# Performance work log

Hardware: AMD Instinct MI355X
Metric: run time of the kernel (lower is better)

Reference implementation:

```python
import jax, jax.numpy as jnp
import numpy as np

H = 128       # hidden size
IN = 6        # input size
OUT = 1       # output size
B, T = 128, 2048


def setup_inputs() -> dict:
    key = jax.random.key(0)
    ks = jax.random.split(key, 16)
    s = 1.0 / np.sqrt(H)  # PyTorch LSTM init: U(-1/sqrt(H), 1/sqrt(H))
    u = lambda k, shape: jax.random.uniform(k, shape, jnp.float32, -s, s)
    inp = {"x": jax.random.normal(ks[0], (B, T, IN), jnp.float32)}
    in_sizes = [IN, H, H]
    for l in range(3):
        inp[f"W_ih{l}"] = u(ks[1 + 4 * l], (4 * H, in_sizes[l]))
        inp[f"W_hh{l}"] = u(ks[2 + 4 * l], (4 * H, H))
        inp[f"b_ih{l}"] = u(ks[3 + 4 * l], (4 * H,))
        inp[f"b_hh{l}"] = u(ks[4 + 4 * l], (4 * H,))
    inp["W_out"] = u(ks[13], (OUT, H))
    inp["b_out"] = u(ks[14], (OUT,))
    return inp


def _lstm_layer(x, W_ih, W_hh, b):
    # x: [B, T, D_in]; precompute input contribution once, scan the recurrence.
    xg = jnp.einsum("bti,gi->btg", x, W_ih) + b  # [B, T, 4H]
    h0 = jnp.zeros((x.shape[0], H), x.dtype)
    c0 = jnp.zeros((x.shape[0], H), x.dtype)

    def step(carry, xg_t):
        h, c = carry
        g = xg_t + h @ W_hh.T                     # [B, 4H]
        i, f, gg, o = jnp.split(g, 4, axis=-1)    # PyTorch gate order i,f,g,o
        i = jax.nn.sigmoid(i)
        f = jax.nn.sigmoid(f)
        gg = jnp.tanh(gg)
        o = jax.nn.sigmoid(o)
        c = f * c + i * gg
        h = o * jnp.tanh(c)
        return (h, c), h

    _, hs = jax.lax.scan(step, (h0, c0), jnp.swapaxes(xg, 0, 1))  # hs: [T, B, H]
    return jnp.swapaxes(hs, 0, 1)


def reference(x, W_ih0, W_hh0, b_ih0, b_hh0, W_ih1, W_hh1, b_ih1, b_hh1,
              W_ih2, W_hh2, b_ih2, b_hh2, W_out, b_out):
    # 3-layer LSTM (dropout inactive in eval mode) + linear head on last step.
    h = _lstm_layer(x, W_ih0, W_hh0, b_ih0 + b_hh0)
    h = _lstm_layer(h, W_ih1, W_hh1, b_ih1 + b_hh1)
    h = _lstm_layer(h, W_ih2, W_hh2, b_ih2 + b_hh2)
    return h[:, -1, :] @ W_out.T + b_out  # [B, 1]
```

## Files before the change

### kernel.cpp

```cpp
#include <hip/hip_runtime.h>

#define B_ 128
#define T_ 2048
#define H_ 128
#define IN_ 6
#define GRP_ 8
#define NGRP_ (T_ / GRP_)
#define CHUNK_ 32
#define NCHUNK_ (T_ / CHUNK_)
#define FLAG_STRIDE_ 64
#define HS_ 144
#define XGRING_ 3
#define XGSLOT_ (CHUNK_ * 8192)

typedef _Float16 f16x8 __attribute__((ext_vector_type(8)));
typedef float    f32x4 __attribute__((ext_vector_type(4)));

__device__ __forceinline__ unsigned short f2h_u(float f) {
  union { _Float16 h; unsigned short u; } v; v.h = (_Float16)f; return v.u;
}
__device__ __forceinline__ unsigned int pack2(float a, float b) {
  return (unsigned int)f2h_u(a) | ((unsigned int)f2h_u(b) << 16);
}
__device__ __forceinline__ float sigf_(float x) {
  return __builtin_amdgcn_rcpf(1.0f + __expf(-x));
}
__device__ __forceinline__ float tanhf_(float x) {
  return 2.0f * __builtin_amdgcn_rcpf(1.0f + __expf(-2.0f * x)) - 1.0f;
}
__device__ __forceinline__ f16x8 load_w8(const float* __restrict__ p) {
  f16x8 r;
#pragma unroll
  for (int i = 0; i < 8; ++i) r[i] = (_Float16)p[i];
  return r;
}

__global__ void init_flags(unsigned int* flags) {
  flags[blockIdx.x * 256 + threadIdx.x] = 0u;
}

__global__ __launch_bounds__(512, 2)
void lstm_pipe(const float* __restrict__ x,
               const float* __restrict__ Wih0, const float* __restrict__ Whh0,
               const float* __restrict__ bih0, const float* __restrict__ bhh0,
               const float* __restrict__ Wih1, const float* __restrict__ Whh1,
               const float* __restrict__ bih1, const float* __restrict__ bhh1,
               const float* __restrict__ Wih2, const float* __restrict__ Whh2,
               const float* __restrict__ bih2, const float* __restrict__ bhh2,
               unsigned short* __restrict__ region,
               float* __restrict__ xg,
               unsigned int* __restrict__ state_h,
               unsigned int* __restrict__ flags)
{
  const int bid  = blockIdx.x;
  const int tid  = threadIdx.x;
  const int lane = tid & 63;
  const int wv   = tid >> 6;
  const int n16  = lane & 15;
  const int quad = lane >> 4;
  const int bcol = n16 & 7;
  const int hh   = n16 >> 3;

  __shared__ unsigned short smem[32 * 16 * HS_];
  __shared__ int s_have;

#define WAITP(ptr_, need_, have_)                                   \
  do {                                                              \
    if ((have_) < (need_)) {                                        \
      if (tid == 0) {                                               \
        int v = (int)__hip_atomic_load(ptr_, __ATOMIC_RELAXED,      \
                                       __HIP_MEMORY_SCOPE_AGENT);   \
        while (v < (need_)) {                                       \
          __builtin_amdgcn_s_sleep(2);                              \
          v = (int)__hip_atomic_load(ptr_, __ATOMIC_RELAXED,        \
                                     __HIP_MEMORY_SCOPE_AGENT);     \
        }                                                           \
        (void)__hip_atomic_load(ptr_, __ATOMIC_ACQUIRE,             \
                                __HIP_MEMORY_SCOPE_AGENT);          \
        s_have = v;                                                 \
      }                                                             \
      __syncthreads();                                              \
      (have_) = s_have;                                             \
    }                                                               \
  } while (0)

  if (bid >= 48) {
    const int gi = bid - 48;
    const int gl = 1 + (gi >> 3);
    const int bg = gi & 7;
    const float* Wih = (gl == 1) ? Wih1 : Wih2;
    const float* bih = (gl == 1) ? bih1 : bih2;
    const float* bhh = (gl == 1) ? bhh1 : bhh2;
    float* xgo = xg + (size_t)((gl - 1) * 8 + bg) * (XGRING_ * (size_t)XGSLOT_);
    unsigned int* fhA = &flags[((gl - 1) * 16 + 2 * bg)     * FLAG_STRIDE_];
    unsigned int* fhB = &flags[((gl - 1) * 16 + 2 * bg + 1) * FLAG_STRIDE_];
    unsigned int* fx_out = &flags[(32 + (gl - 1) * 8 + bg) * FLAG_STRIDE_];
    unsigned int* fcA = &flags[(48 + (gl - 1) * 16 + 2 * bg)     * FLAG_STRIDE_];
    unsigned int* fcB = &flags[(48 + (gl - 1) * 16 + 2 * bg + 1) * FLAG_STRIDE_];

    f16x8 wih[4][4];
#pragma unroll
    for (int j = 0; j < 4; ++j)
#pragma unroll
      for (int kc = 0; kc < 4; ++kc)
        wih[j][kc] = load_w8(Wih + (size_t)(j * 128 + 16 * wv + n16) * H_ + kc * 32 + quad * 8);
    f32x4 bias4[4];
#pragma unroll
    for (int j = 0; j < 4; ++j)
#pragma unroll
      for (int r = 0; r < 4; ++r) {
        int row = j * 128 + 16 * wv + quad * 4 + r;
        bias4[j][r] = bih[row] + bhh[row];
      }

    int haveA = 0, haveB = 0, havecA = 0, havecB = 0;
    const int tt = tid >> 4, bb = tid & 15;
    const int swk = bb & 7;
    for (int k = 0; k < NCHUNK_; ++k) {
      WAITP(fhA, k + 1, haveA);
      WAITP(fhB, k + 1, haveB);
      if (k >= XGRING_) {
        WAITP(fcA, k - (XGRING_ - 1), havecA);
        WAITP(fcB, k - (XGRING_ - 1), havecB);
      }
      {
        const uint4* gp = (const uint4*)(region +
            ((size_t)(bg * 16 + bb) * T_ + (size_t)(CHUNK_ * k + tt)) * H_);
        uint4* lp = (uint4*)&smem[(tt * 16 + bb) * HS_];
#pragma unroll
        for (int i = 0; i < 16; ++i) lp[i ^ swk] = gp[i];
      }
      __syncthreads();
      const int slot = k % XGRING_;
      for (int t = 0; t < CHUNK_; ++t) {
        f16x8 hi[4];
#pragma unroll
        for (int kc = 0; kc < 4; ++kc)
          hi[kc] = *(const f16x8*)&smem[(t * 16 + n16) * HS_ +
                                        ((kc * 32 + quad * 8) ^ (bcol << 3))];
        float* xp = xgo + (size_t)(slot * CHUNK_ + t) * 8192 + quad * 64 + n16 * 4;
#pragma unroll
        for (int j = 0; j < 4; ++j) {
          f32x4 a = bias4[j];
#pragma unroll
          for (int kc = 0; kc < 4; ++kc)
            a = __builtin_amdgcn_mfma_f32_16x16x32_f16(wih[j][kc], hi[kc], a, 0, 0, 0);
          *(f32x4*)(xp + (size_t)(8 * j + wv) * 256) = a;
        }
      }
      __syncthreads();
      if (tid == 0)
        __hip_atomic_store(fx_out, (unsigned int)(k + 1),
                           __ATOMIC_RELEASE, __HIP_MEMORY_SCOPE_AGENT);
    }
    return;
  }

  const int layer = bid >> 4;
  const int bgg   = bid & 15;
  const int bg    = bgg >> 1;
  const int half  = bgg & 1;
  const int batch = bg * 16 + half * 8 + bcol;
  const float* Whh = (layer == 0) ? Whh0 : ((layer == 1) ? Whh1 : Whh2);

  unsigned short* hstate = smem;
  unsigned short* xb = smem + 2 * 8 * HS_;

  f16x8 whh[4][4];
#pragma unroll
  for (int j = 0; j < 4; ++j)
#pragma unroll
    for (int kc = 0; kc < 4; ++kc)
      whh[j][kc] = load_w8(Whh + (size_t)(j * 128 + 16 * wv + n16) * H_ + kc * 32 + quad * 8);

  for (int i = tid; i < (2 * 8 * HS_) / 2; i += 512) ((unsigned int*)smem)[i] = 0u;

  float c20 = 0.f, c21 = 0.f;
  unsigned int dh[GRP_];
  unsigned int* fh_out = (layer < 2) ? &flags[(layer * 16 + bgg) * FLAG_STRIDE_] : nullptr;
  const int hu_idx = (8 * wv + 2 * quad + hh) ^ (bcol << 2);
  const int hcol   = 16 * wv + 4 * quad + 2 * hh;

  if (layer == 0) {
    f32x4 bias4[4];
#pragma unroll
    for (int j = 0; j < 4; ++j)
#pragma unroll
      for (int r = 0; r < 4; ++r) {
        int row = j * 128 + 16 * wv + quad * 4 + r;
        bias4[j][r] = bih0[row] + bhh0[row];
      }
    f16x8 wx[4];
#pragma unroll
    for (int j = 0; j < 4; ++j)
#pragma unroll
      for (int i = 0; i < 8; ++i) wx[j][i] = (_Float16)0.f;
    if (quad == 0) {
#pragma unroll
      for (int j = 0; j < 4; ++j) {
        const float* p = Wih0 + (size_t)(j * 128 + 16 * wv + n16) * IN_;
#pragma unroll
        for (int i = 0; i < IN_; ++i) wx[j][i] = (_Float16)p[i];
      }
    }
    const f32x4 z4 = {0.f, 0.f, 0.f, 0.f};
    const int sn_x = tid & 7, st_x = tid >> 3;
    uint4 xreg = {0u, 0u, 0u, 0u};
    __syncthreads();
    if (tid < 64) {
      const float* xp = x + ((size_t)(bg * 16 + half * 8 + sn_x) * T_ + st_x) * IN_;
      xreg.x = pack2(xp[0], xp[1]); xreg.y = pack2(xp[2], xp[3]);
      xreg.z = pack2(xp[4], xp[5]); xreg.w = 0u;
      *(uint4*)&xb[(st_x * 8 + sn_x) * 8] = xreg;
    }
    __syncthreads();

    for (int g = 0; g < NGRP_; ++g) {
      int gs = (g + 1 < NGRP_) ? (g + 1) : g;
      if (tid < 64) {
        const float* xp = x + ((size_t)(bg * 16 + half * 8 + sn_x) * T_ + (8 * gs + st_x)) * IN_;
        xreg.x = pack2(xp[0], xp[1]); xreg.y = pack2(xp[2], xp[3]);
        xreg.z = pack2(xp[4], xp[5]); xreg.w = 0u;
      }
#pragma unroll
      for (int s = 0; s < GRP_; ++s) {
        const int rp = s & 1, wp = rp ^ 1;
        f16x8 hs[4];
#pragma unroll
        for (int kc = 0; kc < 4; ++kc)
          hs[kc] = *(const f16x8*)&hstate[(rp * 8 + bcol) * HS_ +
                                          ((kc * 32 + quad * 8) ^ (bcol << 3))];
        f16x8 xi;
#pragma unroll
        for (int i = 0; i < 8; ++i) xi[i] = (_Float16)0.f;
        if (quad == 0) xi = *(const f16x8*)&xb[(s * 8 + bcol) * 8];
        f32x4 acc[4];
#pragma unroll
        for (int j = 0; j < 4; ++j) {
          f32x4 aw = bias4[j];
#pragma unroll
          for (int kc = 0; kc < 4; ++kc)
            aw = __builtin_amdgcn_mfma_f32_16x16x32_f16(whh[j][kc], hs[kc], aw, 0, 0, 0);
          f32x4 ai = __builtin_amdgcn_mfma_f32_16x16x32_f16(wx[j], xi, z4, 0, 0, 0);
#pragma unroll
          for (int r = 0; r < 4; ++r) acc[j][r] = aw[r] + ai[r];
        }
        float ga[4], gb[4];
#pragma unroll
        for (int j = 0; j < 4; ++j) {
          ga[j] = hh ? acc[j][2] : acc[j][0];
          gb[j] = hh ? acc[j][3] : acc[j][1];
        }
        float i0 = sigf_(ga[0]), f0 = sigf_(ga[1]), t0 = tanhf_(ga[2]), o0 = sigf_(ga[3]);
        c20 = f0 * c20 + i0 * t0;
        float h0 = o0 * tanhf_(c20);
        float i1 = sigf_(gb[0]), f1 = sigf_(gb[1]), t1 = tanhf_(gb[2]), o1 = sigf_(gb[3]);
        c21 = f1 * c21 + i1 * t1;
        float h1 = o1 * tanhf_(c21);
        unsigned int u = pack2(h0, h1);
        dh[s] = u;
        ((unsigned int*)&hstate[(wp * 8 + bcol) * HS_])[hu_idx] = u;
        __syncthreads();
      }
#pragma unroll
      for (int s = 0; s < GRP_; ++s) {
        size_t off = ((size_t)batch * T_ + (8 * g + s)) * H_ + hcol;
        *(unsigned int*)(region + off) = dh[s];
      }
      if (tid < 64) *(uint4*)&xb[(st_x * 8 + sn_x) * 8] = xreg;
      __syncthreads();
      if (((g & 3) == 3) && tid == 0)
        __hip_atomic_store(fh_out, (unsigned int)((g >> 2) + 1),
                           __ATOMIC_RELEASE, __HIP_MEMORY_SCOPE_AGENT);
    }
  } else {
    const float* xgi = xg + (size_t)((layer - 1) * 8 + bg) * (XGRING_ * (size_t)XGSLOT_);
    const int xcol = half * 8 + bcol;
    f32x4 xr[2][4];
    auto load_xg = [&](int t, int buf) {
      int slot = (t >> 5) % XGRING_;
      const float* p = xgi + (size_t)(slot * CHUNK_ + (t & 31)) * 8192
                       + (size_t)wv * 256 + quad * 64 + xcol * 4;
      xr[buf][0] = *(const f32x4*)(p);
      xr[buf][1] = *(const f32x4*)(p + 2048);
      xr[buf][2] = *(const f32x4*)(p + 4096);
      xr[buf][3] = *(const f32x4*)(p + 6144);
    };
    unsigned int* fx_in  = &flags[(32 + (layer - 1) * 8 + bg) * FLAG_STRIDE_];
    unsigned int* fc_out = &flags[(48 + (layer - 1) * 16 + bgg) * FLAG_STRIDE_];
    int have_x = 0;
    __syncthreads();

    for (int g = 0; g < NGRP_; ++g) {
      if ((g & 3) == 0) {
        int c = g >> 2;
        WAITP(fx_in, c + 1, have_x);
        load_xg(32 * c, 0);
        load_xg(32 * c + 1, 1);
      }
#pragma unroll
      for (int s = 0; s < GRP_; ++s) {
        const int t = 8 * g + s;
        const int rp = s & 1, wp = rp ^ 1;
        f16x8 hs[4];
#pragma unroll
        for (int kc = 0; kc < 4; ++kc)
          hs[kc] = *(const f16x8*)&hstate[(rp * 8 + bcol) * HS_ +
                                          ((kc * 32 + quad * 8) ^ (bcol << 3))];
        f32x4 ci[4];
#pragma unroll
        for (int j = 0; j < 4; ++j) ci[j] = xr[s & 1][j];
        if (!(((g & 3) == 3) && s >= 6)) load_xg(t + 2, s & 1);
        f32x4 acc[4];
#pragma unroll
        for (int j = 0; j < 4; ++j) {
          f32x4 aw = ci[j];
#pragma unroll
          for (int kc = 0; kc < 4; ++kc)
            aw = __builtin_amdgcn_mfma_f32_16x16x32_f16(whh[j][kc], hs[kc], aw, 0, 0, 0);
          acc[j] = aw;
        }
        float ga[4], gb[4];
#pragma unroll
        for (int j = 0; j < 4; ++j) {
          ga[j] = hh ? acc[j][2] : acc[j][0];
          gb[j] = hh ? acc[j][3] : acc[j][1];
        }
        float i0 = sigf_(ga[0]), f0 = sigf_(ga[1]), t0 = tanhf_(ga[2]), o0 = sigf_(ga[3]);
        c20 = f0 * c20 + i0 * t0;
        float h0 = o0 * tanhf_(c20);
        float i1 = sigf_(gb[0]), f1 = sigf_(gb[1]), t1 = tanhf_(gb[2]), o1 = sigf_(gb[3]);
        c21 = f1 * c21 + i1 * t1;
        float h1 = o1 * tanhf_(c21);
        unsigned int u = pack2(h0, h1);
        dh[s] = u;
        ((unsigned int*)&hstate[(wp * 8 + bcol) * HS_])[hu_idx] = u;
        __syncthreads();
      }
      if (layer == 1) {
#pragma unroll
        for (int s = 0; s < GRP_; ++s) {
          size_t off = ((size_t)batch * T_ + (8 * g + s)) * H_ + hcol;
          *(unsigned int*)(region + off) = dh[s];
        }
        __syncthreads();
      }
      if (((g & 3) == 3) && tid == 0) {
        unsigned int cdone = (unsigned int)((g >> 2) + 1);
        if (layer == 1)
          __hip_atomic_store(fh_out, cdone, __ATOMIC_RELEASE, __HIP_MEMORY_SCOPE_AGENT);
        __hip_atomic_store(fc_out, cdone, __ATOMIC_RELEASE, __HIP_MEMORY_SCOPE_AGENT);
      }
    }
    if (layer == 2)
      state_h[(size_t)batch * 64 + (8 * wv + 2 * quad + hh)] = dh[GRP_ - 1];
  }
#undef WAITP
}

__global__ void head_kernel(const unsigned int* __restrict__ state_h,
                            const float* __restrict__ Wout,
                            const float* __restrict__ bout,
                            float* __restrict__ out)
{
  int b = threadIdx.x;
  float s = bout[0];
  for (int j = 0; j < 64; ++j) {
    unsigned int p = state_h[b * 64 + j];
    union { unsigned short u; _Float16 h; } lo, hi;
    lo.u = (unsigned short)(p & 0xffffu);
    hi.u = (unsigned short)(p >> 16);
    s += (float)lo.h * Wout[2 * j] + (float)hi.h * Wout[2 * j + 1];
  }
  out[b] = s;
}

extern "C" void kernel_launch(void* const* d_in, const int* in_sizes, int n_in,
                              void* d_out, int out_size, void* d_ws, size_t ws_size,
                              hipStream_t stream)
{
  const float* x = (const float*)d_in[0];
  const float* Wih[3] = {(const float*)d_in[1], (const float*)d_in[5], (const float*)d_in[9]};
  const float* Whh[3] = {(const float*)d_in[2], (const float*)d_in[6], (const float*)d_in[10]};
  const float* bih[3] = {(const float*)d_in[3], (const float*)d_in[7], (const float*)d_in[11]};
  const float* bhh[3] = {(const float*)d_in[4], (const float*)d_in[8], (const float*)d_in[12]};
  const float* Wout = (const float*)d_in[13];
  const float* bout = (const float*)d_in[14];
  float* out = (float*)d_out;

  char* ws = (char*)d_ws;
  size_t off = 0;
  unsigned short* region = (unsigned short*)(ws + off); off += (size_t)B_ * T_ * H_ * 2;
  float* xg = (float*)(ws + off);                       off += (size_t)16 * XGRING_ * XGSLOT_ * 4;
  unsigned int* state_h  = (unsigned int*)(ws + off);   off += (size_t)B_ * 64 * 4;
  off = (off + 255) & ~(size_t)255;
  unsigned int* flags    = (unsigned int*)(ws + off);   off += 80 * FLAG_STRIDE_ * 4;

  init_flags<<<20, 256, 0, stream>>>(flags);
  lstm_pipe<<<64, 512, 0, stream>>>(x,
      Wih[0], Whh[0], bih[0], bhh[0],
      Wih[1], Whh[1], bih[1], bhh[1],
      Wih[2], Whh[2], bih[2], bhh[2],
      region, xg, state_h, flags);
  head_kernel<<<1, 128, 0, stream>>>(state_h, Wout, bout, out);
}
```

Baseline: 1.790 ms.

## Split recurrent batch into 4-sample slices across twice as many blocks

Each recurrent block now handles 4 batch rows instead of 8, so the 48 recurrent blocks become 96 (32 per layer). Each lane now computes one hidden unit instead of two, which halves per-step gate math and the serial latency per step. The step barriers are replaced with a raw lgkmcnt wait plus s_barrier, and an explicit vmcnt fence is added before flag publication. Layer 0 also folds the input MFMA into the accumulation chain as its first term. In exchange the MFMA tiles are only a quarter used on the batch dimension, there are more flags to poll, and more blocks compete for CUs.

Result: faster. 1.541 ms (-13.9%).

```diff
diff --git a/kernel.cpp b/kernel.cpp
--- a/kernel.cpp
+++ b/kernel.cpp
@@ -12,6 +12,8 @@
 #define HS_ 144
 #define XGRING_ 3
 #define XGSLOT_ (CHUNK_ * 8192)
+#define NSLICE_ 32
+#define NFLAGS_ 144
 
 typedef _Float16 f16x8 __attribute__((ext_vector_type(8)));
 typedef float    f32x4 __attribute__((ext_vector_type(4)));
@@ -38,6 +40,19 @@
 __global__ void init_flags(unsigned int* flags) {
   flags[blockIdx.x * 256 + threadIdx.x] = 0u;
 }
+
+#define BARRIER_LGKM()                                              \
+  do {                                                              \
+    asm volatile("s_waitcnt lgkmcnt(0)" ::: "memory");              \
+    __builtin_amdgcn_s_barrier();                                   \
+    __builtin_amdgcn_sched_barrier(0);                              \
+  } while (0)
+
+#define PUBLISH_FENCE()                                             \
+  do {                                                              \
+    asm volatile("s_waitcnt vmcnt(0)" ::: "memory");                \
+    __builtin_amdgcn_s_barrier();                                   \
+  } while (0)
 
 __global__ __launch_bounds__(512, 2)
 void lstm_pipe(const float* __restrict__ x,
@@ -58,8 +73,6 @@
   const int wv   = tid >> 6;
   const int n16  = lane & 15;
   const int quad = lane >> 4;
-  const int bcol = n16 & 7;
-  const int hh   = n16 >> 3;
 
   __shared__ unsigned short smem[32 * 16 * HS_];
   __shared__ int s_have;
@@ -84,19 +97,22 @@
     }                                                               \
   } while (0)
 
-  if (bid >= 48) {
-    const int gi = bid - 48;
+  if (bid >= 96) {
+    const int gi = bid - 96;
     const int gl = 1 + (gi >> 3);
     const int bg = gi & 7;
+    const int b8 = n16 & 7;
     const float* Wih = (gl == 1) ? Wih1 : Wih2;
     const float* bih = (gl == 1) ? bih1 : bih2;
     const float* bhh = (gl == 1) ? bhh1 : bhh2;
     float* xgo = xg + (size_t)((gl - 1) * 8 + bg) * (XGRING_ * (size_t)XGSLOT_);
-    unsigned int* fhA = &flags[((gl - 1) * 16 + 2 * bg)     * FLAG_STRIDE_];
-    unsigned int* fhB = &flags[((gl - 1) * 16 + 2 * bg + 1) * FLAG_STRIDE_];
-    unsigned int* fx_out = &flags[(32 + (gl - 1) * 8 + bg) * FLAG_STRIDE_];
-    unsigned int* fcA = &flags[(48 + (gl - 1) * 16 + 2 * bg)     * FLAG_STRIDE_];
-    unsigned int* fcB = &flags[(48 + (gl - 1) * 16 + 2 * bg + 1) * FLAG_STRIDE_];
+    unsigned int* fhp[4]; unsigned int* fcp[4];
+#pragma unroll
+    for (int q = 0; q < 4; ++q) {
+      fhp[q] = &flags[((gl - 1) * 32 + 4 * bg + q) * FLAG_STRIDE_];
+      fcp[q] = &flags[(80 + (gl - 1) * 32 + 4 * bg + q) * FLAG_STRIDE_];
+    }
+    unsigned int* fx_out = &flags[(64 + (gl - 1) * 8 + bg) * FLAG_STRIDE_];
 
     f16x8 wih[4][4];
 #pragma unroll
@@ -113,15 +129,20 @@
         bias4[j][r] = bih[row] + bhh[row];
       }
 
-    int haveA = 0, haveB = 0, havecA = 0, havecB = 0;
+    int haveh0 = 0, haveh1 = 0, haveh2 = 0, haveh3 = 0;
+    int havec0 = 0, havec1 = 0, havec2 = 0, havec3 = 0;
     const int tt = tid >> 4, bb = tid & 15;
     const int swk = bb & 7;
     for (int k = 0; k < NCHUNK_; ++k) {
-      WAITP(fhA, k + 1, haveA);
-      WAITP(fhB, k + 1, haveB);
+      WAITP(fhp[0], k + 1, haveh0);
+      WAITP(fhp[1], k + 1, haveh1);
+      WAITP(fhp[2], k + 1, haveh2);
+      WAITP(fhp[3], k + 1, haveh3);
       if (k >= XGRING_) {
-        WAITP(fcA, k - (XGRING_ - 1), havecA);
-        WAITP(fcB, k - (XGRING_ - 1), havecB);
+        WAITP(fcp[0], k - (XGRING_ - 1), havec0);
+        WAITP(fcp[1], k - (XGRING_ - 1), havec1);
+        WAITP(fcp[2], k - (XGRING_ - 1), havec2);
+        WAITP(fcp[3], k - (XGRING_ - 1), havec3);
       }
       {
         const uint4* gp = (const uint4*)(region +
@@ -137,7 +158,7 @@
 #pragma unroll
         for (int kc = 0; kc < 4; ++kc)
           hi[kc] = *(const f16x8*)&smem[(t * 16 + n16) * HS_ +
-                                        ((kc * 32 + quad * 8) ^ (bcol << 3))];
+                                        ((kc * 32 + quad * 8) ^ (b8 << 3))];
         float* xp = xgo + (size_t)(slot * CHUNK_ + t) * 8192 + quad * 64 + n16 * 4;
 #pragma unroll
         for (int j = 0; j < 4; ++j) {
@@ -156,15 +177,15 @@
     return;
   }
 
-  const int layer = bid >> 4;
-  const int bgg   = bid & 15;
-  const int bg    = bgg >> 1;
-  const int half  = bgg & 1;
-  const int batch = bg * 16 + half * 8 + bcol;
+  const int layer = bid >> 5;
+  const int sl    = bid & 31;
+  const int bcol  = n16 & 3;
+  const int rr    = n16 >> 2;
+  const int batch = sl * 4 + bcol;
   const float* Whh = (layer == 0) ? Whh0 : ((layer == 1) ? Whh1 : Whh2);
 
   unsigned short* hstate = smem;
-  unsigned short* xb = smem + 2 * 8 * HS_;
+  unsigned short* xb = smem + 2 * 4 * HS_;
 
   f16x8 whh[4][4];
 #pragma unroll
@@ -173,13 +194,15 @@
     for (int kc = 0; kc < 4; ++kc)
       whh[j][kc] = load_w8(Whh + (size_t)(j * 128 + 16 * wv + n16) * H_ + kc * 32 + quad * 8);
 
-  for (int i = tid; i < (2 * 8 * HS_) / 2; i += 512) ((unsigned int*)smem)[i] = 0u;
-
-  float c20 = 0.f, c21 = 0.f;
-  unsigned int dh[GRP_];
-  unsigned int* fh_out = (layer < 2) ? &flags[(layer * 16 + bgg) * FLAG_STRIDE_] : nullptr;
-  const int hu_idx = (8 * wv + 2 * quad + hh) ^ (bcol << 2);
-  const int hcol   = 16 * wv + 4 * quad + 2 * hh;
+  for (int i = tid; i < (2 * 4 * HS_) / 2; i += 512) ((unsigned int*)smem)[i] = 0u;
+
+  float cc_ = 0.f;
+  unsigned short dh16[GRP_];
+  const bool r2 = (rr & 2) != 0, r1 = (rr & 1) != 0;
+  const int hcol = 16 * wv + 4 * quad + rr;
+  const int s_i  = hcol;
+  const int wswz = (((s_i >> 3) ^ bcol) << 3) | (s_i & 7);
+  unsigned int* fh_out = (layer < 2) ? &flags[(layer * 32 + sl) * FLAG_STRIDE_] : nullptr;
 
   if (layer == 0) {
     f32x4 bias4[4];
@@ -203,24 +226,25 @@
         for (int i = 0; i < IN_; ++i) wx[j][i] = (_Float16)p[i];
       }
     }
-    const f32x4 z4 = {0.f, 0.f, 0.f, 0.f};
-    const int sn_x = tid & 7, st_x = tid >> 3;
-    uint4 xreg = {0u, 0u, 0u, 0u};
+    const int sn_x = tid & 3, st_x = tid >> 2;
+    float xraw[6];
     __syncthreads();
-    if (tid < 64) {
-      const float* xp = x + ((size_t)(bg * 16 + half * 8 + sn_x) * T_ + st_x) * IN_;
-      xreg.x = pack2(xp[0], xp[1]); xreg.y = pack2(xp[2], xp[3]);
-      xreg.z = pack2(xp[4], xp[5]); xreg.w = 0u;
-      *(uint4*)&xb[(st_x * 8 + sn_x) * 8] = xreg;
+    if (tid < 32) {
+      const float* xp = x + ((size_t)(sl * 4 + sn_x) * T_ + st_x) * IN_;
+#pragma unroll
+      for (int i = 0; i < IN_; ++i) xraw[i] = xp[i];
+      uint4 xr4;
+      xr4.x = pack2(xraw[0], xraw[1]); xr4.y = pack2(xraw[2], xraw[3]);
+      xr4.z = pack2(xraw[4], xraw[5]); xr4.w = 0u;
+      *(uint4*)&xb[(st_x * 4 + sn_x) * 8] = xr4;
     }
     __syncthreads();
 
     for (int g = 0; g < NGRP_; ++g) {
-      int gs = (g + 1 < NGRP_) ? (g + 1) : g;
-      if (tid < 64) {
-        const float* xp = x + ((size_t)(bg * 16 + half * 8 + sn_x) * T_ + (8 * gs + st_x)) * IN_;
-        xreg.x = pack2(xp[0], xp[1]); xreg.y = pack2(xp[2], xp[3]);
-        xreg.z = pack2(xp[4], xp[5]); xreg.w = 0u;
+      if (tid < 32 && g + 1 < NGRP_) {
+        const float* xp = x + ((size_t)(sl * 4 + sn_x) * T_ + (8 * (g + 1) + st_x)) * IN_;
+#pragma unroll
+        for (int i = 0; i < IN_; ++i) xraw[i] = xp[i];
       }
 #pragma unroll
       for (int s = 0; s < GRP_; ++s) {
@@ -228,54 +252,57 @@
         f16x8 hs[4];
 #pragma unroll
         for (int kc = 0; kc < 4; ++kc)
-          hs[kc] = *(const f16x8*)&hstate[(rp * 8 + bcol) * HS_ +
+          hs[kc] = *(const f16x8*)&hstate[(rp * 4 + bcol) * HS_ +
                                           ((kc * 32 + quad * 8) ^ (bcol << 3))];
         f16x8 xi;
 #pragma unroll
         for (int i = 0; i < 8; ++i) xi[i] = (_Float16)0.f;
-        if (quad == 0) xi = *(const f16x8*)&xb[(s * 8 + bcol) * 8];
+        if (quad == 0) xi = *(const f16x8*)&xb[(s * 4 + bcol) * 8];
         f32x4 acc[4];
 #pragma unroll
         for (int j = 0; j < 4; ++j) {
-          f32x4 aw = bias4[j];
+          f32x4 a = __builtin_amdgcn_mfma_f32_16x16x32_f16(wx[j], xi, bias4[j], 0, 0, 0);
 #pragma unroll
           for (int kc = 0; kc < 4; ++kc)
-            aw = __builtin_amdgcn_mfma_f32_16x16x32_f16(whh[j][kc], hs[kc], aw, 0, 0, 0);
-          f32x4 ai = __builtin_amdgcn_mfma_f32_16x16x32_f16(wx[j], xi, z4, 0, 0, 0);
-#pragma unroll
-          for (int r = 0; r < 4; ++r) acc[j][r] = aw[r] + ai[r];
-        }
-        float ga[4], gb[4];
+            a = __builtin_amdgcn_mfma_f32_16x16x32_f16(whh[j][kc], hs[kc], a, 0, 0, 0);
+          acc[j] = a;
+        }
+        float g4[4];
 #pragma unroll
         for (int j = 0; j < 4; ++j) {
-          ga[j] = hh ? acc[j][2] : acc[j][0];
-          gb[j] = hh ? acc[j][3] : acc[j][1];
-        }
-        float i0 = sigf_(ga[0]), f0 = sigf_(ga[1]), t0 = tanhf_(ga[2]), o0 = sigf_(ga[3]);
-        c20 = f0 * c20 + i0 * t0;
-        float h0 = o0 * tanhf_(c20);
-        float i1 = sigf_(gb[0]), f1 = sigf_(gb[1]), t1 = tanhf_(gb[2]), o1 = sigf_(gb[3]);
-        c21 = f1 * c21 + i1 * t1;
-        float h1 = o1 * tanhf_(c21);
-        unsigned int u = pack2(h0, h1);
-        dh[s] = u;
-        ((unsigned int*)&hstate[(wp * 8 + bcol) * HS_])[hu_idx] = u;
-        __syncthreads();
-      }
-#pragma unroll
-      for (int s = 0; s < GRP_; ++s) {
-        size_t off = ((size_t)batch * T_ + (8 * g + s)) * H_ + hcol;
-        *(unsigned int*)(region + off) = dh[s];
-      }
-      if (tid < 64) *(uint4*)&xb[(st_x * 8 + sn_x) * 8] = xreg;
-      __syncthreads();
-      if (((g & 3) == 3) && tid == 0)
-        __hip_atomic_store(fh_out, (unsigned int)((g >> 2) + 1),
-                           __ATOMIC_RELEASE, __HIP_MEMORY_SCOPE_AGENT);
+          float t0 = r2 ? acc[j][2] : acc[j][0];
+          float t1 = r2 ? acc[j][3] : acc[j][1];
+          g4[j] = r1 ? t1 : t0;
+        }
+        float i_ = sigf_(g4[0]), f_ = sigf_(g4[1]), t_ = tanhf_(g4[2]), o_ = sigf_(g4[3]);
+        cc_ = f_ * cc_ + i_ * t_;
+        float h_ = o_ * tanhf_(cc_);
+        unsigned short uh = f2h_u(h_);
+        dh16[s] = uh;
+        hstate[(wp * 4 + bcol) * HS_ + wswz] = uh;
+        BARRIER_LGKM();
+      }
+#pragma unroll
+      for (int s = 0; s < GRP_; ++s)
+        region[((size_t)batch * T_ + (8 * g + s)) * H_ + hcol] = dh16[s];
+      if (tid < 32 && g + 1 < NGRP_) {
+        uint4 xr4;
+        xr4.x = pack2(xraw[0], xraw[1]); xr4.y = pack2(xraw[2], xraw[3]);
+        xr4.z = pack2(xraw[4], xraw[5]); xr4.w = 0u;
+        *(uint4*)&xb[(st_x * 4 + sn_x) * 8] = xr4;
+      }
+      BARRIER_LGKM();
+      if ((g & 3) == 3) {
+        PUBLISH_FENCE();
+        if (tid == 0)
+          __hip_atomic_store(fh_out, (unsigned int)((g >> 2) + 1),
+                             __ATOMIC_RELEASE, __HIP_MEMORY_SCOPE_AGENT);
+      }
     }
   } else {
+    const int bg = sl >> 2;
     const float* xgi = xg + (size_t)((layer - 1) * 8 + bg) * (XGRING_ * (size_t)XGSLOT_);
-    const int xcol = half * 8 + bcol;
+    const int xcol = (sl & 3) * 4 + bcol;
     f32x4 xr[2][4];
     auto load_xg = [&](int t, int buf) {
       int slot = (t >> 5) % XGRING_;
@@ -286,8 +313,8 @@
       xr[buf][2] = *(const f32x4*)(p + 4096);
       xr[buf][3] = *(const f32x4*)(p + 6144);
     };
-    unsigned int* fx_in  = &flags[(32 + (layer - 1) * 8 + bg) * FLAG_STRIDE_];
-    unsigned int* fc_out = &flags[(48 + (layer - 1) * 16 + bgg) * FLAG_STRIDE_];
+    unsigned int* fx_in  = &flags[(64 + (layer - 1) * 8 + bg) * FLAG_STRIDE_];
+    unsigned int* fc_out = &flags[(80 + (layer - 1) * 32 + sl) * FLAG_STRIDE_];
     int have_x = 0;
     __syncthreads();
 
@@ -305,7 +332,7 @@
         f16x8 hs[4];
 #pragma unroll
         for (int kc = 0; kc < 4; ++kc)
-          hs[kc] = *(const f16x8*)&hstate[(rp * 8 + bcol) * HS_ +
+          hs[kc] = *(const f16x8*)&hstate[(rp * 4 + bcol) * HS_ +
                                           ((kc * 32 + quad * 8) ^ (bcol << 3))];
         f32x4 ci[4];
 #pragma unroll
@@ -314,46 +341,44 @@
         f32x4 acc[4];
 #pragma unroll
         for (int j = 0; j < 4; ++j) {
-          f32x4 aw = ci[j];
+          f32x4 a = ci[j];
 #pragma unroll
           for (int kc = 0; kc < 4; ++kc)
-            aw = __builtin_amdgcn_mfma_f32_16x16x32_f16(whh[j][kc], hs[kc], aw, 0, 0, 0);
-          acc[j] = aw;
-        }
-        float ga[4], gb[4];
+            a = __builtin_amdgcn_mfma_f32_16x16x32_f16(whh[j][kc], hs[kc], a, 0, 0, 0);
+          acc[j] = a;
+        }
+        float g4[4];
 #pragma unroll
         for (int j = 0; j < 4; ++j) {
-          ga[j] = hh ? acc[j][2] : acc[j][0];
-          gb[j] = hh ? acc[j][3] : acc[j][1];
-        }
-        float i0 = sigf_(ga[0]), f0 = sigf_(ga[1]), t0 = tanhf_(ga[2]), o0 = sigf_(ga[3]);
-        c20 = f0 * c20 + i0 * t0;
-        float h0 = o0 * tanhf_(c20);
-        float i1 = sigf_(gb[0]), f1 = sigf_(gb[1]), t1 = tanhf_(gb[2]), o1 = sigf_(gb[3]);
-        c21 = f1 * c21 + i1 * t1;
-        float h1 = o1 * tanhf_(c21);
-        unsigned int u = pack2(h0, h1);
-        dh[s] = u;
-        ((unsigned int*)&hstate[(wp * 8 + bcol) * HS_])[hu_idx] = u;
-        __syncthreads();
+          float t0 = r2 ? acc[j][2] : acc[j][0];
+          float t1 = r2 ? acc[j][3] : acc[j][1];
+          g4[j] = r1 ? t1 : t0;
+        }
+        float i_ = sigf_(g4[0]), f_ = sigf_(g4[1]), t_ = tanhf_(g4[2]), o_ = sigf_(g4[3]);
+        cc_ = f_ * cc_ + i_ * t_;
+        float h_ = o_ * tanhf_(cc_);
+        unsigned short uh = f2h_u(h_);
+        dh16[s] = uh;
+        hstate[(wp * 4 + bcol) * HS_ + wswz] = uh;
+        BARRIER_LGKM();
       }
       if (layer == 1) {
 #pragma unroll
-        for (int s = 0; s < GRP_; ++s) {
-          size_t off = ((size_t)batch * T_ + (8 * g + s)) * H_ + hcol;
-          *(unsigned int*)(region + off) = dh[s];
-        }
-        __syncthreads();
-      }
-      if (((g & 3) == 3) && tid == 0) {
-        unsigned int cdone = (unsigned int)((g >> 2) + 1);
-        if (layer == 1)
-          __hip_atomic_store(fh_out, cdone, __ATOMIC_RELEASE, __HIP_MEMORY_SCOPE_AGENT);
-        __hip_atomic_store(fc_out, cdone, __ATOMIC_RELEASE, __HIP_MEMORY_SCOPE_AGENT);
+        for (int s = 0; s < GRP_; ++s)
+          region[((size_t)batch * T_ + (8 * g + s)) * H_ + hcol] = dh16[s];
+      }
+      if ((g & 3) == 3) {
+        PUBLISH_FENCE();
+        if (tid == 0) {
+          unsigned int cdone = (unsigned int)((g >> 2) + 1);
+          if (layer == 1)
+            __hip_atomic_store(fh_out, cdone, __ATOMIC_RELEASE, __HIP_MEMORY_SCOPE_AGENT);
+          __hip_atomic_store(fc_out, cdone, __ATOMIC_RELEASE, __HIP_MEMORY_SCOPE_AGENT);
+        }
       }
     }
     if (layer == 2)
-      state_h[(size_t)batch * 64 + (8 * wv + 2 * quad + hh)] = dh[GRP_ - 1];
+      ((unsigned short*)state_h)[(size_t)batch * 128 + hcol] = dh16[GRP_ - 1];
   }
 #undef WAITP
 }
@@ -394,10 +419,10 @@
   float* xg = (float*)(ws + off);                       off += (size_t)16 * XGRING_ * XGSLOT_ * 4;
   unsigned int* state_h  = (unsigned int*)(ws + off);   off += (size_t)B_ * 64 * 4;
   off = (off + 255) & ~(size_t)255;
-  unsigned int* flags    = (unsigned int*)(ws + off);   off += 80 * FLAG_STRIDE_ * 4;
-
-  init_flags<<<20, 256, 0, stream>>>(flags);
-  lstm_pipe<<<64, 512, 0, stream>>>(x,
+  unsigned int* flags    = (unsigned int*)(ws + off);   off += NFLAGS_ * FLAG_STRIDE_ * 4;
+
+  init_flags<<<36, 256, 0, stream>>>(flags);
+  lstm_pipe<<<112, 512, 0, stream>>>(x,
       Wih[0], Whh[0], bih[0], bhh[0],
       Wih[1], Whh[1], bih[1], bhh[1],
       Wih[2], Whh[2], bih[2], bhh[2],
```
